# Optimization experiments

Measured on AMD Instinct MI355X. Metric: run time of the kernel, lower is better.

Reference implementation:

```python
import jax, jax.numpy as jnp
import numpy as np
from jax.scipy.linalg import solve_triangular

JITTER = 1e-4  # settings.jitter
N, NUM_NODES, DIN, DOUT, M, DEG = 2048, 64, 4, 4, 128, 8
P = DEG * DIN  # parent-feature width per node


def _rbf(a, b):
    # unit-variance, unit-lengthscale RBF kernel: [Na, D] x [Nb, D] -> [Na, Nb]
    sq = (jnp.sum(a * a, -1)[:, None] + jnp.sum(b * b, -1)[None, :]
          - 2.0 * (a @ b.T))
    return jnp.exp(-0.5 * jnp.maximum(sq, 0.0))


def setup_inputs() -> dict:
    key = jax.random.key(0)
    k1, k2, k3, k4 = jax.random.split(key, 4)
    X = jax.random.normal(k1, (N, NUM_NODES * DIN), jnp.float32)
    Z = jax.random.normal(k2, (M, NUM_NODES * DIN), jnp.float32)
    q_mu = 0.1 * jax.random.normal(k3, (M, NUM_NODES * DOUT), jnp.float32)
    q_sqrt = (0.05 * jax.random.normal(k4, (NUM_NODES, DOUT, M, M), jnp.float32)
              + jnp.eye(M, dtype=jnp.float32))
    # fixed-degree graph: parents of node nd are (nd+k) % NUM_NODES, k<DEG;
    # pa[nd] holds the DIN contiguous feature columns of each parent (as in pa_idx)
    parents = (np.arange(NUM_NODES)[:, None] + np.arange(DEG)[None, :]) % NUM_NODES
    cols = (parents[:, :, None] * DIN + np.arange(DIN)[None, None, :]).reshape(NUM_NODES, P)
    pa = jnp.asarray(cols, dtype=jnp.int32)
    return {"X": X, "Z": Z, "q_mu": q_mu, "q_sqrt": q_sqrt, "pa": pa}


def reference(X, Z, q_mu, q_sqrt, pa):
    num_nodes, dout, m, _ = q_sqrt.shape
    n = X.shape[0]
    eye = jnp.eye(m, dtype=X.dtype)
    # q_mu columns per node: [M, nodes*Dout] -> [nodes, M, Dout]
    q_mu_n = q_mu.reshape(m, num_nodes, dout).transpose(1, 0, 2)

    def per_node(pa_nd, qmu_nd, qs_nd):
        Zn = Z[:, pa_nd]             # [M, P]
        Xn = X[:, pa_nd]             # [N, P]
        Ku = _rbf(Zn, Zn) + JITTER * eye
        Lu = jnp.linalg.cholesky(Ku)
        Kuf = _rbf(Zn, Xn)           # [M, N]
        A = solve_triangular(Lu, Kuf, lower=True)
        A = solve_triangular(Lu.T, A, lower=False)   # Kuu^{-1} Kuf, [M, N]
        mean = A.T @ qmu_nd          # [N, Dout] (Zero mean function)
        Lq = jnp.tril(qs_nd)         # [Dout, M, M]
        SK = jnp.einsum('dij,dkj->dik', Lq, Lq) - Ku[None]  # S - Kuu
        B = jnp.einsum('dmk,kn->dmn', SK, A)                 # [Dout, M, N]
        delta = jnp.einsum('mn,dmn->dn', A, B)               # [Dout, N]
        var = 1.0 + delta.T          # Kdiag of unit-variance RBF is 1
        return mean, var

    mean, var = jax.vmap(per_node)(pa, q_mu_n, q_sqrt)   # [nodes, N, Dout]
    mean = mean.transpose(1, 0, 2).reshape(n, num_nodes * dout)
    var = var.transpose(1, 0, 2).reshape(n, num_nodes * dout)
    return mean, var
```

## Files before the change

### kernel.cpp

```cpp
#include <hip/hip_runtime.h>
#include <hip/hip_bf16.h>

#define NN      2048
#define NODES   64
#define DIN     4
#define DOUT    4
#define MM      128
#define DEG     8
#define PP      32
#define JITTER  1e-4f

typedef __attribute__((ext_vector_type(8))) short short8;
typedef __attribute__((ext_vector_type(4))) float f32x4;
typedef __attribute__((ext_vector_type(4))) unsigned short bf16x4;

#define HSTRIDE 81920

__device__ __forceinline__ unsigned short f2b(float f) {
    union { float f; unsigned int u; } v; v.f = f;
    unsigned int u = v.u;
    u += 0x7fffu + ((u >> 16) & 1u);
    return (unsigned short)(u >> 16);
}
__device__ __forceinline__ float b2f(unsigned short h) {
    union { unsigned int u; float f; } v; v.u = ((unsigned int)h) << 16;
    return v.f;
}
__device__ __forceinline__ short8 pack8(f32x4 a, f32x4 b, float& sq) {
    short8 r;
    #pragma unroll
    for (int e = 0; e < 4; e++) {
        unsigned short ha = f2b(a[e]), hb = f2b(b[e]);
        float fa = b2f(ha), fb = b2f(hb);
        sq += fa * fa + fb * fb;
        r[e] = (short)ha; r[e + 4] = (short)hb;
    }
    return r;
}

__device__ __forceinline__ void gload16(const unsigned short* g, unsigned short* l) {
    __builtin_amdgcn_global_load_lds(
        (const __attribute__((address_space(1))) unsigned int*)g,
        (__attribute__((address_space(3))) unsigned int*)l, 16, 0, 0);
}

__global__ __launch_bounds__(512) void k_nsgt(const float* __restrict__ Z,
                                              const int* __restrict__ pa,
                                              const float* __restrict__ qmu,
                                              const float* __restrict__ qsqrt,
                                              unsigned short* __restrict__ Wbf,
                                              unsigned short* __restrict__ Hbuf,
                                              unsigned short* __restrict__ Zpan,
                                              float* __restrict__ zsqg) {
    __shared__ unsigned short SA[16384];
    __shared__ unsigned short SB[16384];
    __shared__ float zsqs[128];
    __shared__ int cols[32];
    int bid = blockIdx.x, t = threadIdx.x;
    int node = (bid & 7) + 8 * (bid >> 5);
    int d = (bid >> 3) & 3;
    int wv = t >> 6, ln = t & 63;
    if (t < 32) cols[t] = pa[node * 32 + t];
    __syncthreads();

    int wmI = wv & 1, wnI = wv >> 1;
    int wm = wmI * 64, wn = wnI * 32;
    int lr = ln & 15, lk = ln >> 4;
    int cg0 = cols[lk * 8], cg1 = cols[lk * 8 + 4];

    short8 zv[4], xv[2];
    #pragma unroll
    for (int mi = 0; mi < 4; mi++) {
        int m = wm + mi * 16 + lr;
        float sq = 0.f;
        zv[mi] = pack8(*(const f32x4*)(Z + (size_t)m * 256 + cg0),
                       *(const f32x4*)(Z + (size_t)m * 256 + cg1), sq);
        sq += __shfl_xor(sq, 16);
        sq += __shfl_xor(sq, 32);
        if (lk == 0) zsqs[m] = sq;
        if (d == 0 && wnI == 0)
            *(short8*)(Zpan + (size_t)node * 4096 + (size_t)m * 32 + lk * 8) = zv[mi];
    }
    #pragma unroll
    for (int ni = 0; ni < 2; ni++) {
        int x = wn + ni * 16 + lr;
        float sq = 0.f;
        xv[ni] = pack8(*(const f32x4*)(Z + (size_t)x * 256 + cg0),
                       *(const f32x4*)(Z + (size_t)x * 256 + cg1), sq);
    }
    __syncthreads();
    if (d == 0 && t < 128) zsqg[node * 128 + t] = zsqs[t];

    f32x4 dacc[4][2] = {};
    #pragma unroll
    for (int mi = 0; mi < 4; mi++)
        #pragma unroll
        for (int ni = 0; ni < 2; ni++)
            dacc[mi][ni] = __builtin_amdgcn_mfma_f32_16x16x32_bf16(zv[mi], xv[ni], dacc[mi][ni], 0, 0, 0);

    #pragma unroll
    for (int mi = 0; mi < 4; mi++) {
        int mb = wm + mi * 16 + lk * 4;
        f32x4 zs4 = *(const f32x4*)(zsqs + mb);
        #pragma unroll
        for (int ni = 0; ni < 2; ni++) {
            int x = wn + ni * 16 + lr;
            float xs = zsqs[x];
            bf16x4 kv4;
            #pragma unroll
            for (int j = 0; j < 4; j++) {
                float sq = fmaxf(zs4[j] + xs - 2.0f * dacc[mi][ni][j], 0.0f);
                float v = (mb + j == x) ? JITTER : __expf(-0.5f * sq);
                kv4[j] = f2b(v);
            }
            *(bf16x4*)(SA + x * 128 + (((mb >> 3) ^ (x & 7)) * 8) + (mb & 7)) = kv4;
        }
    }
    __syncthreads();

    f32x4 acc1[4][2] = {};
    #pragma unroll
    for (int ks = 0; ks < 4; ks++) {
        int seg = ks * 4 + lk;
        short8 av[4], bv[2];
        #pragma unroll
        for (int mi = 0; mi < 4; mi++) {
            int r = wm + mi * 16 + lr;
            av[mi] = *(const short8*)(SA + r * 128 + ((seg ^ (r & 7)) * 8));
        }
        #pragma unroll
        for (int ni = 0; ni < 2; ni++) {
            int x = wn + ni * 16 + lr;
            bv[ni] = *(const short8*)(SA + x * 128 + ((seg ^ (x & 7)) * 8));
        }
        #pragma unroll
        for (int mi = 0; mi < 4; mi++)
            #pragma unroll
            for (int ni = 0; ni < 2; ni++)
                acc1[mi][ni] = __builtin_amdgcn_mfma_f32_16x16x32_bf16(av[mi], bv[ni], acc1[mi][ni], 0, 0, 0);
    }
    #pragma unroll
    for (int mi = 0; mi < 4; mi++)
        #pragma unroll
        for (int ni = 0; ni < 2; ni++)
            #pragma unroll
            for (int j = 0; j < 4; j++) {
                int rr = wm + mi * 16 + lk * 4 + j;
                int cc = wn + ni * 16 + lr;
                SB[rr * 128 + (((cc >> 3) ^ (rr & 7)) * 8) + (cc & 7)] = f2b(acc1[mi][ni][j]);
            }
    __syncthreads();

    f32x4 acc2[4][2] = {};
    #pragma unroll
    for (int ks = 0; ks < 4; ks++) {
        int seg = ks * 4 + lk;
        short8 av[4], bv[2];
        #pragma unroll
        for (int mi = 0; mi < 4; mi++) {
            int r = wm + mi * 16 + lr;
            av[mi] = *(const short8*)(SA + r * 128 + ((seg ^ (r & 7)) * 8));
        }
        #pragma unroll
        for (int ni = 0; ni < 2; ni++) {
            int x = wn + ni * 16 + lr;
            bv[ni] = *(const short8*)(SB + x * 128 + ((seg ^ (x & 7)) * 8));
        }
        #pragma unroll
        for (int mi = 0; mi < 4; mi++)
            #pragma unroll
            for (int ni = 0; ni < 2; ni++)
                acc2[mi][ni] = __builtin_amdgcn_mfma_f32_16x16x32_bf16(av[mi], bv[ni], acc2[mi][ni], 0, 0, 0);
    }
    __syncthreads();

    unsigned short* Hr = Hbuf + (size_t)node * HSTRIDE + 65536;
    #pragma unroll
    for (int mi = 0; mi < 4; mi++)
        #pragma unroll
        for (int ni = 0; ni < 2; ni++)
            #pragma unroll
            for (int j = 0; j < 4; j++) {
                int rr = wm + mi * 16 + lk * 4 + j;
                int cc = wn + ni * 16 + lr;
                int sw = rr * 128 + (((cc >> 3) ^ (rr & 7)) * 8) + (cc & 7);
                float dv = b2f(SA[sw]);
                float eye = (rr == cc) ? 1.0f : 0.0f;
                float s1 = acc1[mi][ni][j], s2 = acc2[mi][ni][j];
                float kinv = eye - dv + s1 - s2;
                float rv = eye - 0.5f * dv + 0.375f * s1 - 0.3125f * s2;
                SA[sw] = f2b(kinv);
                if (d == 0) Hr[sw] = f2b(rv);
            }
    if (d == 0) {
        for (int q = t; q < 2048; q += 512) {
            int dd = q >> 7, mm = q & 127;
            unsigned short val = 0;
            if (dd < 4) val = f2b(qmu[mm * 256 + node * 4 + dd]);
            SB[dd * 128 + (((mm >> 3) ^ (dd & 7)) * 8) + (mm & 7)] = val;
        }
    }
    __syncthreads();

    if (d == 0) {
        f32x4 wacc = {};
        #pragma unroll
        for (int ks = 0; ks < 4; ks++) {
            int seg = ks * 4 + lk;
            short8 aq = *(const short8*)(SB + lr * 128 + ((seg ^ (lr & 7)) * 8));
            int x = wv * 16 + lr;
            short8 bk = *(const short8*)(SA + x * 128 + ((seg ^ (x & 7)) * 8));
            wacc = __builtin_amdgcn_mfma_f32_16x16x32_bf16(aq, bk, wacc, 0, 0, 0);
        }
        unsigned short* Wg = Wbf + (size_t)node * 2048;
        #pragma unroll
        for (int j = 0; j < 4; j++) {
            int dd = lk * 4 + j;
            int mm = wv * 16 + lr;
            Wg[dd * 128 + (((mm >> 3) ^ (dd & 7)) * 8) + (mm & 7)] = f2b(wacc[j]);
        }
    }
    __syncthreads();

    {
        const float* Lq = qsqrt + (size_t)(node * 4 + d) * 16384;
        int m = t & 127, ph = t >> 7;
        for (int pp = 0; pp < 32; pp++) {
            int p = ph * 32 + pp;
            float v = 0.f;
            if (p >= m) v = Lq[p * 128 + m];
            SB[m * 128 + (((p >> 3) ^ (m & 7)) * 8) + (p & 7)] = f2b(v);
        }
    }
    __syncthreads();

    f32x4 gacc[4][2] = {};
    #pragma unroll
    for (int ks = 0; ks < 4; ks++) {
        int seg = ks * 4 + lk;
        short8 av[4], bv[2];
        #pragma unroll
        for (int mi = 0; mi < 4; mi++) {
            int r = wm + mi * 16 + lr;
            av[mi] = *(const short8*)(SB + r * 128 + ((seg ^ (r & 7)) * 8));
        }
        #pragma unroll
        for (int ni = 0; ni < 2; ni++) {
            int x = wn + ni * 16 + lr;
            bv[ni] = *(const short8*)(SA + x * 128 + ((seg ^ (x & 7)) * 8));
        }
        #pragma unroll
        for (int mi = 0; mi < 4; mi++)
            #pragma unroll
            for (int ni = 0; ni < 2; ni++)
                gacc[mi][ni] = __builtin_amdgcn_mfma_f32_16x16x32_bf16(av[mi], bv[ni], gacc[mi][ni], 0, 0, 0);
    }
    unsigned short* Gg = Hbuf + (size_t)node * HSTRIDE + (size_t)d * 16384;
    #pragma unroll
    for (int mi = 0; mi < 4; mi++)
        #pragma unroll
        for (int ni = 0; ni < 2; ni++)
            #pragma unroll
            for (int j = 0; j < 4; j++) {
                int rr = wm + mi * 16 + lk * 4 + j;
                int cc = wn + ni * 16 + lr;
                Gg[rr * 128 + (((cc >> 3) ^ (rr & 7)) * 8) + (cc & 7)] = f2b(gacc[mi][ni][j]);
            }
}

__global__ __launch_bounds__(512, 1) void k_main(const float* __restrict__ X,
                                                 const unsigned short* __restrict__ Zpan,
                                                 const float* __restrict__ zsqg,
                                                 const int* __restrict__ pa,
                                                 const unsigned short* __restrict__ Hbuf,
                                                 const unsigned short* __restrict__ Wbf,
                                                 float* __restrict__ out) {
    __shared__ unsigned short A0[16384];
    __shared__ unsigned short A1[16384];

    int bid = blockIdx.x;
    int node = (bid & 7) + 8 * (bid >> 6);
    int half = (bid >> 3) & 7;
    int x0 = half * 256;
    int t = threadIdx.x;
    int wv = t >> 6, ln = t & 63;
    int lr = ln & 15, lk = ln >> 4;

    const unsigned short* Asrc = Hbuf + (size_t)node * HSTRIDE;
    const unsigned short* Wsrc = Wbf + (size_t)node * 2048;
    int cg0 = pa[node * 32 + lk * 8];
    int cg1 = pa[node * 32 + lk * 8 + 4];

    unsigned short* strip = A1 + wv * 2048;

    const unsigned short* Zp = Zpan + (size_t)node * 4096;
    short8 zv[8];
    #pragma unroll
    for (int mi = 0; mi < 8; mi++)
        zv[mi] = *(const short8*)(Zp + (size_t)(mi * 16 + lr) * 32 + lk * 8);
    #pragma unroll
    for (int i = 0; i < 4; i++) {
        int ch = i * 8 + wv;
        gload16(Asrc + ch * 512 + ln * 8, A0 + ch * 512);
    }
    short8 aw[4];
    #pragma unroll
    for (int ks = 0; ks < 4; ks++)
        aw[ks] = *(const short8*)(Wsrc + lr * 128 + (((ks * 4 + lk) ^ (lr & 7)) * 8));

    const float* Xb = X + (size_t)(x0 + wv * 32 + lr) * 256;
    const float* zsq_n = zsqg + node * 128;
    f32x4 xr0 = *(const f32x4*)(Xb + cg0);
    f32x4 xr1 = *(const f32x4*)(Xb + cg1);
    short8 bvAll[2][4];
    f32x4 maccA[2];
    #pragma unroll
    for (int it = 0; it < 2; it++) {
        float xs = 0.f;
        short8 xv = pack8(xr0, xr1, xs);
        xs += __shfl_xor(xs, 16);
        xs += __shfl_xor(xs, 32);
        if (it < 1) {
            xr0 = *(const f32x4*)(Xb + 4096 + cg0);
            xr1 = *(const f32x4*)(Xb + 4096 + cg1);
        }
        f32x4 dacc[8] = {};
        #pragma unroll
        for (int mi = 0; mi < 8; mi++)
            dacc[mi] = __builtin_amdgcn_mfma_f32_16x16x32_bf16(zv[mi], xv, dacc[mi], 0, 0, 0);
        #pragma unroll
        for (int mi = 0; mi < 8; mi++) {
            int mb = mi * 16 + lk * 4;
            f32x4 zs4 = *(const f32x4*)(zsq_n + mb);
            bf16x4 kv4;
            #pragma unroll
            for (int j = 0; j < 4; j++) {
                float sq = fmaxf(zs4[j] + xs - 2.0f * dacc[mi][j], 0.0f);
                kv4[j] = f2b(__expf(-0.5f * sq));
            }
            *(bf16x4*)(strip + lr * 128 + (((mb >> 3) ^ (lr & 7)) * 8) + (mb & 7)) = kv4;
        }
        #pragma unroll
        for (int ks = 0; ks < 4; ks++)
            bvAll[it][ks] = *(const short8*)(strip + lr * 128 + (((ks * 4 + lk) ^ (lr & 7)) * 8));
        f32x4 m4 = {};
        #pragma unroll
        for (int ks = 0; ks < 4; ks++)
            m4 = __builtin_amdgcn_mfma_f32_16x16x32_bf16(aw[ks], bvAll[it][ks], m4, 0, 0, 0);
        maccA[it] = m4;
    }

    float vout[5][2];
    #pragma unroll
    for (int tt = 0; tt < 5; tt++) {
        unsigned short* cbuf = (tt & 1) ? A1 : A0;
        __syncthreads();
        if (tt < 4) {
            const unsigned short* ns = Asrc + (size_t)(tt + 1) * 16384;
            unsigned short* nb = (tt & 1) ? A0 : A1;
            #pragma unroll
            for (int i = 0; i < 4; i++) {
                int ch = i * 8 + wv;
                gload16(ns + ch * 512 + ln * 8, nb + ch * 512);
            }
        }
        float ssum[2] = {0.f, 0.f};
        __builtin_amdgcn_s_setprio(1);
        #pragma unroll
        for (int mi = 0; mi < 8; mi++) {
            int r = mi * 16 + lr;
            f32x4 a4[2] = {};
            #pragma unroll
            for (int ks = 0; ks < 4; ks++) {
                short8 av = *(const short8*)(cbuf + r * 128 + (((ks * 4 + lk) ^ (r & 7)) * 8));
                #pragma unroll
                for (int it = 0; it < 2; it++)
                    a4[it] = __builtin_amdgcn_mfma_f32_16x16x32_bf16(av, bvAll[it][ks], a4[it], 0, 0, 0);
            }
            #pragma unroll
            for (int it = 0; it < 2; it++)
                #pragma unroll
                for (int j = 0; j < 4; j++) ssum[it] += a4[it][j] * a4[it][j];
        }
        __builtin_amdgcn_s_setprio(0);
        #pragma unroll
        for (int it = 0; it < 2; it++) {
            float sv = ssum[it];
            sv += __shfl_xor(sv, 16);
            sv += __shfl_xor(sv, 32);
            vout[tt][it] = sv;
        }
    }

    if (lk == 0) {
        #pragma unroll
        for (int it = 0; it < 2; it++) {
            int x = x0 + wv * 32 + it * 16 + lr;
            f32x4 mv, vv;
            #pragma unroll
            for (int j = 0; j < 4; j++) {
                mv[j] = maccA[it][j];
                vv[j] = 1.0f + vout[j][it] - vout[4][it];
            }
            *(f32x4*)(out + (size_t)x * 256 + node * 4) = mv;
            *(f32x4*)(out + 524288 + (size_t)x * 256 + node * 4) = vv;
        }
    }
}

extern "C" void kernel_launch(void* const* d_in, const int* in_sizes, int n_in,
                              void* d_out, int out_size, void* d_ws, size_t ws_size,
                              hipStream_t stream) {
    const float* X = (const float*)d_in[0];
    const float* Z = (const float*)d_in[1];
    const float* qmu = (const float*)d_in[2];
    const float* qsqrt = (const float*)d_in[3];
    const int* pa = (const int*)d_in[4];
    float* out = (float*)d_out;

    char* ws = (char*)d_ws;
    size_t off = 0;
    unsigned short* Wbf = (unsigned short*)(ws + off);   off += 131072ull * 2;
    unsigned short* Hbuf = (unsigned short*)(ws + off);  off += 5242880ull * 2;
    unsigned short* Zpan = (unsigned short*)(ws + off);  off += 262144ull * 2;
    float* zsqg = (float*)(ws + off);                    off += 8192ull * 4;

    k_nsgt<<<256, 512, 0, stream>>>(Z, pa, qmu, qsqrt, Wbf, Hbuf, Zpan, zsqg);
    k_main<<<512, 512, 0, stream>>>(X, Zpan, zsqg, pa, Hbuf, Wbf, out);
}
```

Before: 57.20 us.

## Precompute per-output M = G·Gᵀ − Kinv so variance uses quadratic form, drop fifth pass

The setup kernel now forms, for each output dimension, M_d = G_d G_dᵀ − Kuu⁻¹ by an extra 128×128 MFMA product per node and stores it in place of the separate G and Kinv-approximation buffers. The main kernel no longer needs the fifth shared Kinv pass. It computes the variance as kᵀ M_d k by multiplying the staged matrix with the kernel column and dotting with the kernel values kept in registers. This removes a fifth of the main-loop MFMA work and one buffered load stage, and shrinks the workspace. The cost is more setup-kernel compute, extra registers for the kernel values, and an extra bf16 rounding of M.

After: 71.59 us. +25.2%, slower.

```diff
diff --git a/kernel.cpp b/kernel.cpp
--- a/kernel.cpp
+++ b/kernel.cpp
@@ -14,7 +14,7 @@
 typedef __attribute__((ext_vector_type(4))) float f32x4;
 typedef __attribute__((ext_vector_type(4))) unsigned short bf16x4;
 
-#define HSTRIDE 81920
+#define HSTRIDE 65536
 
 __device__ __forceinline__ unsigned short f2b(float f) {
     union { float f; unsigned int u; } v; v.f = f;
@@ -174,7 +174,6 @@
     }
     __syncthreads();
 
-    unsigned short* Hr = Hbuf + (size_t)node * HSTRIDE + 65536;
     #pragma unroll
     for (int mi = 0; mi < 4; mi++)
         #pragma unroll
@@ -186,11 +185,8 @@
                 int sw = rr * 128 + (((cc >> 3) ^ (rr & 7)) * 8) + (cc & 7);
                 float dv = b2f(SA[sw]);
                 float eye = (rr == cc) ? 1.0f : 0.0f;
-                float s1 = acc1[mi][ni][j], s2 = acc2[mi][ni][j];
-                float kinv = eye - dv + s1 - s2;
-                float rv = eye - 0.5f * dv + 0.375f * s1 - 0.3125f * s2;
+                float kinv = eye - dv + acc1[mi][ni][j] - acc2[mi][ni][j];
                 SA[sw] = f2b(kinv);
-                if (d == 0) Hr[sw] = f2b(rv);
             }
     if (d == 0) {
         for (int q = t; q < 2048; q += 512) {
@@ -255,7 +251,8 @@
             for (int ni = 0; ni < 2; ni++)
                 gacc[mi][ni] = __builtin_amdgcn_mfma_f32_16x16x32_bf16(av[mi], bv[ni], gacc[mi][ni], 0, 0, 0);
     }
-    unsigned short* Gg = Hbuf + (size_t)node * HSTRIDE + (size_t)d * 16384;
+    __syncthreads();
+
     #pragma unroll
     for (int mi = 0; mi < 4; mi++)
         #pragma unroll
@@ -264,7 +261,43 @@
             for (int j = 0; j < 4; j++) {
                 int rr = wm + mi * 16 + lk * 4 + j;
                 int cc = wn + ni * 16 + lr;
-                Gg[rr * 128 + (((cc >> 3) ^ (rr & 7)) * 8) + (cc & 7)] = f2b(gacc[mi][ni][j]);
+                SB[cc * 128 + (((rr >> 3) ^ (cc & 7)) * 8) + (rr & 7)] = f2b(gacc[mi][ni][j]);
+            }
+    __syncthreads();
+
+    f32x4 macc[4][2] = {};
+    #pragma unroll
+    for (int ks = 0; ks < 4; ks++) {
+        int seg = ks * 4 + lk;
+        short8 av[4], bv[2];
+        #pragma unroll
+        for (int mi = 0; mi < 4; mi++) {
+            int r = wm + mi * 16 + lr;
+            av[mi] = *(const short8*)(SB + r * 128 + ((seg ^ (r & 7)) * 8));
+        }
+        #pragma unroll
+        for (int ni = 0; ni < 2; ni++) {
+            int x = wn + ni * 16 + lr;
+            bv[ni] = *(const short8*)(SB + x * 128 + ((seg ^ (x & 7)) * 8));
+        }
+        #pragma unroll
+        for (int mi = 0; mi < 4; mi++)
+            #pragma unroll
+            for (int ni = 0; ni < 2; ni++)
+                macc[mi][ni] = __builtin_amdgcn_mfma_f32_16x16x32_bf16(av[mi], bv[ni], macc[mi][ni], 0, 0, 0);
+    }
+    unsigned short* Mg = Hbuf + (size_t)node * HSTRIDE + (size_t)d * 16384;
+    #pragma unroll
+    for (int mi = 0; mi < 4; mi++)
+        #pragma unroll
+        for (int ni = 0; ni < 2; ni++)
+            #pragma unroll
+            for (int j = 0; j < 4; j++) {
+                int rr = wm + mi * 16 + lk * 4 + j;
+                int cc = wn + ni * 16 + lr;
+                int sw = rr * 128 + (((cc >> 3) ^ (rr & 7)) * 8) + (cc & 7);
+                float mval = macc[mi][ni][j] - b2f(SA[sw]);
+                Mg[sw] = f2b(mval);
             }
 }
 
@@ -313,6 +346,7 @@
     f32x4 xr0 = *(const f32x4*)(Xb + cg0);
     f32x4 xr1 = *(const f32x4*)(Xb + cg1);
     short8 bvAll[2][4];
+    bf16x4 kreg[8][2];
     f32x4 maccA[2];
     #pragma unroll
     for (int it = 0; it < 2; it++) {
@@ -338,6 +372,7 @@
                 float sq = fmaxf(zs4[j] + xs - 2.0f * dacc[mi][j], 0.0f);
                 kv4[j] = f2b(__expf(-0.5f * sq));
             }
+            kreg[mi][it] = kv4;
             *(bf16x4*)(strip + lr * 128 + (((mb >> 3) ^ (lr & 7)) * 8) + (mb & 7)) = kv4;
         }
         #pragma unroll
@@ -350,12 +385,12 @@
         maccA[it] = m4;
     }
 
-    float vout[5][2];
-    #pragma unroll
-    for (int tt = 0; tt < 5; tt++) {
+    float vout[4][2];
+    #pragma unroll
+    for (int tt = 0; tt < 4; tt++) {
         unsigned short* cbuf = (tt & 1) ? A1 : A0;
         __syncthreads();
-        if (tt < 4) {
+        if (tt < 3) {
             const unsigned short* ns = Asrc + (size_t)(tt + 1) * 16384;
             unsigned short* nb = (tt & 1) ? A0 : A1;
             #pragma unroll
@@ -380,7 +415,8 @@
             #pragma unroll
             for (int it = 0; it < 2; it++)
                 #pragma unroll
-                for (int j = 0; j < 4; j++) ssum[it] += a4[it][j] * a4[it][j];
+                for (int j = 0; j < 4; j++)
+                    ssum[it] += a4[it][j] * b2f(kreg[mi][it][j]);
         }
         __builtin_amdgcn_s_setprio(0);
         #pragma unroll
@@ -400,7 +436,7 @@
             #pragma unroll
             for (int j = 0; j < 4; j++) {
                 mv[j] = maccA[it][j];
-                vv[j] = 1.0f + vout[j][it] - vout[4][it];
+                vv[j] = 1.0f + vout[j][it];
             }
             *(f32x4*)(out + (size_t)x * 256 + node * 4) = mv;
             *(f32x4*)(out + 524288 + (size_t)x * 256 + node * 4) = vv;
@@ -421,7 +457,7 @@
     char* ws = (char*)d_ws;
     size_t off = 0;
     unsigned short* Wbf = (unsigned short*)(ws + off);   off += 131072ull * 2;
-    unsigned short* Hbuf = (unsigned short*)(ws + off);  off += 5242880ull * 2;
+    unsigned short* Hbuf = (unsigned short*)(ws + off);  off += 4194304ull * 2;
     unsigned short* Zpan = (unsigned short*)(ws + off);  off += 262144ull * 2;
     float* zsqg = (float*)(ws + off);                    off += 8192ull * 4;
 
```
